# Performance work log

Hardware: AMD Instinct MI355X
Metric: run time of the kernel (lower is better)

The kernel has to match this reference:

```python
import jax, jax.numpy as jnp
import numpy as np

EMBED_DIM = 256
N_HEADS = 8
HEAD_DIM = EMBED_DIM // N_HEADS
SCALE = HEAD_DIM ** -0.5
CLAMP = 50.0


def setup_inputs() -> dict:
    key = jax.random.key(0)
    ks = jax.random.split(key, 5)
    B, R, N, E = 2, 32, 512, EMBED_DIM
    x = jax.random.normal(ks[0], (B, R, N, E), dtype=jnp.float32)
    # key-padding mask, broadcastable to (b, h, i, j): keys >= 448 are masked
    mask = (jnp.arange(N) < 448)[None, None, None, :]
    Wqkv = jax.random.normal(ks[1], (E, 3 * E), dtype=jnp.float32) * (E ** -0.5)
    bqkv = jax.random.normal(ks[2], (3 * E,), dtype=jnp.float32) * 0.02
    Wo = jax.random.normal(ks[3], (E, E), dtype=jnp.float32) * (E ** -0.5)
    bo = jax.random.normal(ks[4], (E,), dtype=jnp.float32) * 0.02
    return {"x": x, "mask": mask, "Wqkv": Wqkv, "bqkv": bqkv, "Wo": Wo, "bo": bo}


def reference(x, mask, Wqkv, bqkv, Wo, bo):
    *lead, n, e = x.shape
    xf = x.reshape(-1, n, e)                        # (b, n, e), b = prod(lead)
    qkv = xf @ Wqkv + bqkv                          # (b, n, 3e)
    q, k, v = jnp.split(qkv, 3, axis=-1)
    def heads(t):                                   # (b, n, e) -> (b, h, n, d)
        return t.reshape(t.shape[0], n, N_HEADS, HEAD_DIM).transpose(0, 2, 1, 3)
    q, k, v = heads(q), heads(k), heads(v)
    attn = jnp.einsum('bhid,bhjd->bhij', q, k) * SCALE
    attn = jnp.clip(attn, -CLAMP, CLAMP)
    attn = jnp.where(mask, attn, -jnp.inf)
    attn = jax.nn.softmax(attn, axis=-1)
    # dropout is identity in eval mode
    out = jnp.einsum('bhij,bhjd->bhid', attn, v)    # (b, h, n, d)
    out = out.transpose(0, 2, 1, 3).reshape(-1, n, e)
    out = out @ Wo + bo
    return out.reshape(*lead, n, e)
```

## Files before the change

kernel.cpp:

```cpp
#include <hip/hip_runtime.h>
#include <hip/hip_bf16.h>


typedef __bf16 bf16x8 __attribute__((ext_vector_type(8)));
typedef float f32x4 __attribute__((ext_vector_type(4)));
typedef __hip_bfloat16 bf16_t;

#define QSCALE 0.2550348762f
#define MAXC   72.13475204444817f

__device__ __forceinline__ bf16_t f2b(float f) { return __float2bfloat16(f); }

__global__ __launch_bounds__(256) void prep_w(
    const float* __restrict__ Wqkv, const float* __restrict__ Wo,
    bf16_t* __restrict__ wq_t, bf16_t* __restrict__ wo_t)
{
    int i = blockIdx.x * 256 + threadIdx.x;
    if (i < 196608) { int n = i >> 8, k = i & 255; wq_t[i] = f2b(Wqkv[k * 768 + n]); }
    else { int j = i - 196608; int n = j >> 8, k = j & 255; wo_t[j] = f2b(Wo[k * 256 + n]); }
}

__global__ __launch_bounds__(256) void qkv_gemm(
    const float* __restrict__ x, const bf16_t* __restrict__ Bt, const float* __restrict__ bias,
    bf16_t* __restrict__ Qp, bf16_t* __restrict__ Kp, bf16_t* __restrict__ Vp)
{
    __shared__ bf16_t smem[2 * 128 * 72];
    bf16_t* As = smem;
    bf16_t* Bs = smem + 128 * 72;
    const int tid = threadIdx.x, lane = tid & 63, w = tid >> 6;
    const int q = lane >> 4, c = lane & 15;
    const int wm = w >> 1, wn = w & 1;
    const int bm0 = blockIdx.x * 128, bn0 = blockIdx.y * 128;

    const f32x4 fz = {0.f, 0.f, 0.f, 0.f};
    f32x4 acc[4][4];
#pragma unroll
    for (int i = 0; i < 4; i++)
#pragma unroll
        for (int j = 0; j < 4; j++) acc[i][j] = fz;

    for (int kk = 0; kk < 4; ++kk) {
        const int k0 = kk * 64;
#pragma unroll
        for (int t = 0; t < 8; t++) {
            int idx = tid + t * 256;
            int row = idx >> 4, c4 = idx & 15;
            float4 f = *(const float4*)&x[(size_t)(bm0 + row) * 256 + k0 + c4 * 4];
            union { ushort4 u; bf16_t h[4]; } pk;
            pk.h[0] = f2b(f.x); pk.h[1] = f2b(f.y); pk.h[2] = f2b(f.z); pk.h[3] = f2b(f.w);
            *(ushort4*)&As[row * 72 + c4 * 4] = pk.u;
        }
#pragma unroll
        for (int t = 0; t < 4; t++) {
            int idx = tid + t * 256;
            int row = idx >> 3, c8 = idx & 7;
            *(uint4*)&Bs[row * 72 + c8 * 8] = *(const uint4*)&Bt[(size_t)(bn0 + row) * 256 + k0 + c8 * 8];
        }
        __syncthreads();
#pragma unroll
        for (int ks = 0; ks < 2; ks++) {
            bf16x8 af[4], bfr[4];
#pragma unroll
            for (int mt = 0; mt < 4; mt++) af[mt] = *(const bf16x8*)&As[(wm * 64 + mt * 16 + c) * 72 + ks * 32 + q * 8];
#pragma unroll
            for (int nt = 0; nt < 4; nt++) bfr[nt] = *(const bf16x8*)&Bs[(wn * 64 + nt * 16 + c) * 72 + ks * 32 + q * 8];
#pragma unroll
            for (int mt = 0; mt < 4; mt++)
#pragma unroll
                for (int nt = 0; nt < 4; nt++)
                    acc[mt][nt] = __builtin_amdgcn_mfma_f32_16x16x32_bf16(af[mt], bfr[nt], acc[mt][nt], 0, 0, 0);
        }
        __syncthreads();
    }

    bf16_t* T = smem + w * 4608;
    const int sel = bn0 >> 8;
    const int npb = bm0 + wm * 64;
    const int bseq = npb >> 9;
    const int blk = (npb & 511) >> 6;
    const int hbase = ((bn0 >> 5) & 7) + wn * 2;

    if (sel == 2) {
#pragma unroll
        for (int mt = 0; mt < 4; mt++)
#pragma unroll
            for (int nt = 0; nt < 4; nt++) {
                int gn = bn0 + wn * 64 + nt * 16 + c;
                float b = bias[gn];
                union { ushort4 u; bf16_t h[4]; } pk;
#pragma unroll
                for (int r = 0; r < 4; r++) pk.h[r] = f2b(acc[mt][nt][r] + b);
                *(ushort4*)&T[(nt * 16 + c) * 72 + mt * 16 + q * 4] = pk.u;
            }
        if (blk < 7) {
#pragma unroll
            for (int t = 0; t < 8; t++) {
                int h = t >> 2, s2 = (t >> 1) & 1, dt = t & 1;
                uint4 vv = *(const uint4*)&T[(h * 32 + dt * 16 + c) * 72 + s2 * 32 + q * 8];
                int bh = bseq * 8 + hbase + h;
                *(uint4*)&Vp[((((size_t)bh * 7 + blk) * 2 + s2) * 2 + dt) * 512 + lane * 8] = vv;
            }
        }
    } else {
        const float sc = (sel == 0) ? QSCALE : 1.0f;
#pragma unroll
        for (int mt = 0; mt < 4; mt++)
#pragma unroll
            for (int nt = 0; nt < 4; nt++) {
                int gn = bn0 + wn * 64 + nt * 16 + c;
                float b = bias[gn];
#pragma unroll
                for (int r = 0; r < 4; r++)
                    T[(mt * 16 + q * 4 + r) * 72 + nt * 16 + c] = f2b((acc[mt][nt][r] + b) * sc);
            }
        if (sel == 0) {
#pragma unroll
            for (int t = 0; t < 8; t++) {
                int h = t >> 2, g = t & 3;
                uint4 vv = *(const uint4*)&T[(g * 16 + c) * 72 + h * 32 + q * 8];
                int bh = bseq * 8 + hbase + h;
                *(uint4*)&Qp[(((size_t)bh * 8 + blk) * 4 + g) * 512 + lane * 8] = vv;
            }
        } else if (blk < 7) {
#pragma unroll
            for (int t = 0; t < 8; t++) {
                int h = t >> 2, g = t & 3;
                uint4 vv = *(const uint4*)&T[(g * 16 + c) * 72 + h * 32 + q * 8];
                int bh = bseq * 8 + hbase + h;
                *(uint4*)&Kp[(((size_t)bh * 7 + blk) * 4 + g) * 512 + lane * 8] = vv;
            }
        }
    }
}

__global__ __launch_bounds__(256) void attn_kernel(
    const bf16_t* __restrict__ Qp, const bf16_t* __restrict__ Kp,
    const bf16_t* __restrict__ Vp, bf16_t* __restrict__ a_buf)
{
    __shared__ bf16_t Pw[4 * 16 * 68];
    const int tid = threadIdx.x, lane = tid & 63, w = tid >> 6;
    const int q = lane >> 4, c = lane & 15;
    const int bh = blockIdx.x & 511, part = blockIdx.x >> 9;
    bf16_t* pw = &Pw[w * 16 * 68];

    bf16x8 Qf = *(const bf16x8*)&Qp[(((size_t)bh * 8 + part) * 4 + w) * 512 + lane * 8];

    union { bf16x8 v; bf16_t h[8]; } ones;
#pragma unroll
    for (int j = 0; j < 8; j++) ones.h[j] = f2b(1.0f);

    const f32x4 fz = {0.f, 0.f, 0.f, 0.f};
    f32x4 O0 = fz, O1 = fz, lacc = fz;

#pragma unroll 1
    for (int ch = 0; ch < 7; ++ch) {
        bf16x8 Kf[4], Vf[4];
#pragma unroll
        for (int nt = 0; nt < 4; nt++)
            Kf[nt] = *(const bf16x8*)&Kp[(((size_t)bh * 7 + ch) * 4 + nt) * 512 + lane * 8];
#pragma unroll
        for (int t = 0; t < 4; t++)
            Vf[t] = *(const bf16x8*)&Vp[(((size_t)bh * 7 + ch) * 4 + t) * 512 + lane * 8];

        f32x4 s[4];
#pragma unroll
        for (int nt = 0; nt < 4; nt++)
            s[nt] = __builtin_amdgcn_mfma_f32_16x16x32_bf16(Qf, Kf[nt], fz, 0, 0, 0);
#pragma unroll
        for (int nt = 0; nt < 4; nt++)
#pragma unroll
            for (int r = 0; r < 4; r++) {
                float t = fminf(s[nt][r] - MAXC, 0.f);
                pw[(q * 4 + r) * 68 + nt * 16 + c] = f2b(__builtin_amdgcn_exp2f(t));
            }
#pragma unroll
        for (int s2 = 0; s2 < 2; s2++) {
            bf16x8 Pa = *(const bf16x8*)&pw[c * 68 + s2 * 32 + q * 8];
            lacc = __builtin_amdgcn_mfma_f32_16x16x32_bf16(Pa, ones.v, lacc, 0, 0, 0);
            O0 = __builtin_amdgcn_mfma_f32_16x16x32_bf16(Pa, Vf[s2 * 2 + 0], O0, 0, 0, 0);
            O1 = __builtin_amdgcn_mfma_f32_16x16x32_bf16(Pa, Vf[s2 * 2 + 1], O1, 0, 0, 0);
        }
    }

    const int bseq = bh >> 3, hh = bh & 7;
#pragma unroll
    for (int r = 0; r < 4; r++) {
        float inv = 1.f / lacc[r];
        int row = part * 64 + w * 16 + q * 4 + r;
        size_t tok = (size_t)bseq * 512 + row;
        a_buf[tok * 256 + hh * 32 + c]      = f2b(O0[r] * inv);
        a_buf[tok * 256 + hh * 32 + 16 + c] = f2b(O1[r] * inv);
    }
}

__global__ __launch_bounds__(256) void out_gemm(
    const bf16_t* __restrict__ A, const bf16_t* __restrict__ Bt, const float* __restrict__ bias,
    float* __restrict__ out)
{
    __shared__ bf16_t As[128 * 72];
    __shared__ bf16_t Bs[64 * 72];
    const int tid = threadIdx.x, lane = tid & 63, w = tid >> 6;
    const int q = lane >> 4, c = lane & 15;
    const int bm0 = blockIdx.x * 128, bn0 = blockIdx.y * 64;

    const f32x4 fz = {0.f, 0.f, 0.f, 0.f};
    f32x4 acc[2][4];
#pragma unroll
    for (int i = 0; i < 2; i++)
#pragma unroll
        for (int j = 0; j < 4; j++) acc[i][j] = fz;

    for (int kk = 0; kk < 4; ++kk) {
        const int k0 = kk * 64;
#pragma unroll
        for (int t = 0; t < 4; t++) {
            int idx = tid + t * 256;
            int row = idx >> 3, c8 = idx & 7;
            *(uint4*)&As[row * 72 + c8 * 8] = *(const uint4*)&A[(size_t)(bm0 + row) * 256 + k0 + c8 * 8];
        }
#pragma unroll
        for (int t = 0; t < 2; t++) {
            int idx = tid + t * 256;
            int row = idx >> 3, c8 = idx & 7;
            *(uint4*)&Bs[row * 72 + c8 * 8] = *(const uint4*)&Bt[(size_t)(bn0 + row) * 256 + k0 + c8 * 8];
        }
        __syncthreads();
#pragma unroll
        for (int ks = 0; ks < 2; ks++) {
            bf16x8 af[2], bfr[4];
#pragma unroll
            for (int mt = 0; mt < 2; mt++) af[mt] = *(const bf16x8*)&As[(w * 32 + mt * 16 + c) * 72 + ks * 32 + q * 8];
#pragma unroll
            for (int nt = 0; nt < 4; nt++) bfr[nt] = *(const bf16x8*)&Bs[(nt * 16 + c) * 72 + ks * 32 + q * 8];
#pragma unroll
            for (int mt = 0; mt < 2; mt++)
#pragma unroll
                for (int nt = 0; nt < 4; nt++)
                    acc[mt][nt] = __builtin_amdgcn_mfma_f32_16x16x32_bf16(af[mt], bfr[nt], acc[mt][nt], 0, 0, 0);
        }
        __syncthreads();
    }
#pragma unroll
    for (int mt = 0; mt < 2; mt++)
#pragma unroll
        for (int nt = 0; nt < 4; nt++) {
            int gn = bn0 + nt * 16 + c;
            float b = bias[gn];
#pragma unroll
            for (int r = 0; r < 4; r++) {
                int gm = bm0 + w * 32 + mt * 16 + q * 4 + r;
                out[(size_t)gm * 256 + gn] = acc[mt][nt][r] + b;
            }
        }
}

extern "C" void kernel_launch(void* const* d_in, const int* in_sizes, int n_in,
                              void* d_out, int out_size, void* d_ws, size_t ws_size,
                              hipStream_t stream)
{
    const float* x    = (const float*)d_in[0];
    const float* Wqkv = (const float*)d_in[2];
    const float* bqkv = (const float*)d_in[3];
    const float* Wo   = (const float*)d_in[4];
    const float* bo   = (const float*)d_in[5];
    float* out = (float*)d_out;

    char* ws = (char*)d_ws;
    bf16_t* Qp    = (bf16_t*)(ws);
    bf16_t* Kp    = (bf16_t*)(ws + 16777216);
    bf16_t* Vp    = (bf16_t*)(ws + 31457280);
    bf16_t* a_buf = (bf16_t*)(ws + 46137344);
    bf16_t* wq_t  = (bf16_t*)(ws + 62914560);
    bf16_t* wo_t  = (bf16_t*)(ws + 63307776);

    prep_w<<<1024, 256, 0, stream>>>(Wqkv, Wo, wq_t, wo_t);
    qkv_gemm<<<dim3(256, 6), 256, 0, stream>>>(x, wq_t, bqkv, Qp, Kp, Vp);
    attn_kernel<<<4096, 256, 0, stream>>>(Qp, Kp, Vp, a_buf);
    out_gemm<<<dim3(256, 4), 256, 0, stream>>>(a_buf, wo_t, bo, out);
}
```

Measured before the change: 171.5 us.

## Fuse output projection into attention kernel with MFMA-fragment-ordered Wo

Merges the attention and output-projection kernels. Each block now handles one sequence's 32 query rows across all 8 heads (two passes of 4 waves), stages the normalized head outputs in shared memory, and runs the Wo GEMM directly from there. Wo is pre-packed in MFMA fragment order so B fragments load straight from global memory. This removes the bf16 a_buf round trip and one kernel launch, but cuts the attention grid from 4096 to 1024 blocks. Each wave now re-reads K/V per head pass and holds two query tiles, which adds register pressure.

```diff
diff --git a/kernel.cpp b/kernel.cpp
--- a/kernel.cpp
+++ b/kernel.cpp
@@ -13,11 +13,18 @@
 
 __global__ __launch_bounds__(256) void prep_w(
     const float* __restrict__ Wqkv, const float* __restrict__ Wo,
-    bf16_t* __restrict__ wq_t, bf16_t* __restrict__ wo_t)
+    bf16_t* __restrict__ wq_t, bf16_t* __restrict__ Wof)
 {
     int i = blockIdx.x * 256 + threadIdx.x;
-    if (i < 196608) { int n = i >> 8, k = i & 255; wq_t[i] = f2b(Wqkv[k * 768 + n]); }
-    else { int j = i - 196608; int n = j >> 8, k = j & 255; wo_t[j] = f2b(Wo[k * 256 + n]); }
+    if (i < 196608) {
+        int n = i >> 8, k = i & 255;
+        wq_t[i] = f2b(Wqkv[k * 768 + n]);
+    } else {
+        int j = i - 196608;
+        int n = j >> 8, k = j & 255;
+        int ks = k >> 5, nt = n >> 4, cc = n & 15, qq = (k >> 3) & 3, jj = k & 7;
+        Wof[(((ks * 16 + nt) * 4 + qq) * 16 + cc) * 8 + jj] = f2b(Wo[k * 256 + n]);
+    }
 }
 
 __global__ __launch_bounds__(256) void qkv_gemm(
@@ -133,123 +140,112 @@
     }
 }
 
-__global__ __launch_bounds__(256) void attn_kernel(
+__global__ __launch_bounds__(256) void attn_fused(
     const bf16_t* __restrict__ Qp, const bf16_t* __restrict__ Kp,
-    const bf16_t* __restrict__ Vp, bf16_t* __restrict__ a_buf)
-{
+    const bf16_t* __restrict__ Vp, const bf16_t* __restrict__ Wof,
+    const float* __restrict__ bo, float* __restrict__ out)
+{
+    __shared__ bf16_t Os[32 * 280];
     __shared__ bf16_t Pw[4 * 16 * 68];
     const int tid = threadIdx.x, lane = tid & 63, w = tid >> 6;
     const int q = lane >> 4, c = lane & 15;
-    const int bh = blockIdx.x & 511, part = blockIdx.x >> 9;
+    const int b = blockIdx.x;
+    const int seq = b & 63, part = b >> 6;
     bf16_t* pw = &Pw[w * 16 * 68];
 
-    bf16x8 Qf = *(const bf16x8*)&Qp[(((size_t)bh * 8 + part) * 4 + w) * 512 + lane * 8];
-
     union { bf16x8 v; bf16_t h[8]; } ones;
 #pragma unroll
     for (int j = 0; j < 8; j++) ones.h[j] = f2b(1.0f);
-
     const f32x4 fz = {0.f, 0.f, 0.f, 0.f};
-    f32x4 O0 = fz, O1 = fz, lacc = fz;
 
 #pragma unroll 1
-    for (int ch = 0; ch < 7; ++ch) {
-        bf16x8 Kf[4], Vf[4];
-#pragma unroll
-        for (int nt = 0; nt < 4; nt++)
-            Kf[nt] = *(const bf16x8*)&Kp[(((size_t)bh * 7 + ch) * 4 + nt) * 512 + lane * 8];
-#pragma unroll
-        for (int t = 0; t < 4; t++)
-            Vf[t] = *(const bf16x8*)&Vp[(((size_t)bh * 7 + ch) * 4 + t) * 512 + lane * 8];
-
-        f32x4 s[4];
-#pragma unroll
-        for (int nt = 0; nt < 4; nt++)
-            s[nt] = __builtin_amdgcn_mfma_f32_16x16x32_bf16(Qf, Kf[nt], fz, 0, 0, 0);
-#pragma unroll
-        for (int nt = 0; nt < 4; nt++)
+    for (int pass = 0; pass < 2; ++pass) {
+        const int head = w + pass * 4;
+        const int bh = seq * 8 + head;
+
+        bf16x8 Qf[2];
+#pragma unroll
+        for (int mt = 0; mt < 2; mt++)
+            Qf[mt] = *(const bf16x8*)&Qp[(((size_t)bh * 8 + (part >> 1)) * 4 + (part & 1) * 2 + mt) * 512 + lane * 8];
+
+        f32x4 O[2][2], lacc[2];
+#pragma unroll
+        for (int mt = 0; mt < 2; mt++) { O[mt][0] = fz; O[mt][1] = fz; lacc[mt] = fz; }
+
+#pragma unroll 1
+        for (int ch = 0; ch < 7; ++ch) {
+            bf16x8 Kf[4], Vf[4];
+#pragma unroll
+            for (int nt = 0; nt < 4; nt++)
+                Kf[nt] = *(const bf16x8*)&Kp[(((size_t)bh * 7 + ch) * 4 + nt) * 512 + lane * 8];
+#pragma unroll
+            for (int t = 0; t < 4; t++)
+                Vf[t] = *(const bf16x8*)&Vp[(((size_t)bh * 7 + ch) * 4 + t) * 512 + lane * 8];
+
+#pragma unroll
+            for (int mt = 0; mt < 2; mt++) {
+                f32x4 s[4];
+#pragma unroll
+                for (int nt = 0; nt < 4; nt++)
+                    s[nt] = __builtin_amdgcn_mfma_f32_16x16x32_bf16(Qf[mt], Kf[nt], fz, 0, 0, 0);
+#pragma unroll
+                for (int nt = 0; nt < 4; nt++)
+#pragma unroll
+                    for (int r = 0; r < 4; r++) {
+                        float t = fminf(s[nt][r] - MAXC, 0.f);
+                        pw[(q * 4 + r) * 68 + nt * 16 + c] = f2b(__builtin_amdgcn_exp2f(t));
+                    }
+#pragma unroll
+                for (int s2 = 0; s2 < 2; s2++) {
+                    bf16x8 Pa = *(const bf16x8*)&pw[c * 68 + s2 * 32 + q * 8];
+                    lacc[mt] = __builtin_amdgcn_mfma_f32_16x16x32_bf16(Pa, ones.v, lacc[mt], 0, 0, 0);
+                    O[mt][0] = __builtin_amdgcn_mfma_f32_16x16x32_bf16(Pa, Vf[s2 * 2 + 0], O[mt][0], 0, 0, 0);
+                    O[mt][1] = __builtin_amdgcn_mfma_f32_16x16x32_bf16(Pa, Vf[s2 * 2 + 1], O[mt][1], 0, 0, 0);
+                }
+            }
+        }
+#pragma unroll
+        for (int mt = 0; mt < 2; mt++)
 #pragma unroll
             for (int r = 0; r < 4; r++) {
-                float t = fminf(s[nt][r] - MAXC, 0.f);
-                pw[(q * 4 + r) * 68 + nt * 16 + c] = f2b(__builtin_amdgcn_exp2f(t));
-            }
-#pragma unroll
-        for (int s2 = 0; s2 < 2; s2++) {
-            bf16x8 Pa = *(const bf16x8*)&pw[c * 68 + s2 * 32 + q * 8];
-            lacc = __builtin_amdgcn_mfma_f32_16x16x32_bf16(Pa, ones.v, lacc, 0, 0, 0);
-            O0 = __builtin_amdgcn_mfma_f32_16x16x32_bf16(Pa, Vf[s2 * 2 + 0], O0, 0, 0, 0);
-            O1 = __builtin_amdgcn_mfma_f32_16x16x32_bf16(Pa, Vf[s2 * 2 + 1], O1, 0, 0, 0);
-        }
-    }
-
-    const int bseq = bh >> 3, hh = bh & 7;
-#pragma unroll
-    for (int r = 0; r < 4; r++) {
-        float inv = 1.f / lacc[r];
-        int row = part * 64 + w * 16 + q * 4 + r;
-        size_t tok = (size_t)bseq * 512 + row;
-        a_buf[tok * 256 + hh * 32 + c]      = f2b(O0[r] * inv);
-        a_buf[tok * 256 + hh * 32 + 16 + c] = f2b(O1[r] * inv);
-    }
-}
-
-__global__ __launch_bounds__(256) void out_gemm(
-    const bf16_t* __restrict__ A, const bf16_t* __restrict__ Bt, const float* __restrict__ bias,
-    float* __restrict__ out)
-{
-    __shared__ bf16_t As[128 * 72];
-    __shared__ bf16_t Bs[64 * 72];
-    const int tid = threadIdx.x, lane = tid & 63, w = tid >> 6;
-    const int q = lane >> 4, c = lane & 15;
-    const int bm0 = blockIdx.x * 128, bn0 = blockIdx.y * 64;
-
-    const f32x4 fz = {0.f, 0.f, 0.f, 0.f};
+                float inv = 1.f / lacc[mt][r];
+                int row = mt * 16 + q * 4 + r;
+                Os[row * 280 + head * 32 + c]      = f2b(O[mt][0][r] * inv);
+                Os[row * 280 + head * 32 + 16 + c] = f2b(O[mt][1][r] * inv);
+            }
+    }
+    __syncthreads();
+
     f32x4 acc[2][4];
 #pragma unroll
     for (int i = 0; i < 2; i++)
 #pragma unroll
         for (int j = 0; j < 4; j++) acc[i][j] = fz;
 
-    for (int kk = 0; kk < 4; ++kk) {
-        const int k0 = kk * 64;
-#pragma unroll
-        for (int t = 0; t < 4; t++) {
-            int idx = tid + t * 256;
-            int row = idx >> 3, c8 = idx & 7;
-            *(uint4*)&As[row * 72 + c8 * 8] = *(const uint4*)&A[(size_t)(bm0 + row) * 256 + k0 + c8 * 8];
-        }
-#pragma unroll
-        for (int t = 0; t < 2; t++) {
-            int idx = tid + t * 256;
-            int row = idx >> 3, c8 = idx & 7;
-            *(uint4*)&Bs[row * 72 + c8 * 8] = *(const uint4*)&Bt[(size_t)(bn0 + row) * 256 + k0 + c8 * 8];
-        }
-        __syncthreads();
-#pragma unroll
-        for (int ks = 0; ks < 2; ks++) {
-            bf16x8 af[2], bfr[4];
-#pragma unroll
-            for (int mt = 0; mt < 2; mt++) af[mt] = *(const bf16x8*)&As[(w * 32 + mt * 16 + c) * 72 + ks * 32 + q * 8];
-#pragma unroll
-            for (int nt = 0; nt < 4; nt++) bfr[nt] = *(const bf16x8*)&Bs[(nt * 16 + c) * 72 + ks * 32 + q * 8];
+#pragma unroll
+    for (int ks = 0; ks < 8; ++ks) {
+        bf16x8 af[2];
+#pragma unroll
+        for (int mt = 0; mt < 2; mt++)
+            af[mt] = *(const bf16x8*)&Os[(mt * 16 + c) * 280 + ks * 32 + q * 8];
+#pragma unroll
+        for (int nt = 0; nt < 4; nt++) {
+            bf16x8 bfr = *(const bf16x8*)&Wof[(((size_t)ks * 16 + w * 4 + nt) * 64 + lane) * 8];
 #pragma unroll
             for (int mt = 0; mt < 2; mt++)
-#pragma unroll
-                for (int nt = 0; nt < 4; nt++)
-                    acc[mt][nt] = __builtin_amdgcn_mfma_f32_16x16x32_bf16(af[mt], bfr[nt], acc[mt][nt], 0, 0, 0);
-        }
-        __syncthreads();
+                acc[mt][nt] = __builtin_amdgcn_mfma_f32_16x16x32_bf16(af[mt], bfr, acc[mt][nt], 0, 0, 0);
+        }
     }
 #pragma unroll
     for (int mt = 0; mt < 2; mt++)
 #pragma unroll
         for (int nt = 0; nt < 4; nt++) {
-            int gn = bn0 + nt * 16 + c;
-            float b = bias[gn];
+            int gn = w * 64 + nt * 16 + c;
+            float bb = bo[gn];
 #pragma unroll
             for (int r = 0; r < 4; r++) {
-                int gm = bm0 + w * 32 + mt * 16 + q * 4 + r;
-                out[(size_t)gm * 256 + gn] = acc[mt][nt][r] + b;
+                int gm = seq * 512 + part * 32 + mt * 16 + q * 4 + r;
+                out[(size_t)gm * 256 + gn] = acc[mt][nt][r] + bb;
             }
         }
 }
@@ -266,15 +262,13 @@
     float* out = (float*)d_out;
 
     char* ws = (char*)d_ws;
-    bf16_t* Qp    = (bf16_t*)(ws);
-    bf16_t* Kp    = (bf16_t*)(ws + 16777216);
-    bf16_t* Vp    = (bf16_t*)(ws + 31457280);
-    bf16_t* a_buf = (bf16_t*)(ws + 46137344);
-    bf16_t* wq_t  = (bf16_t*)(ws + 62914560);
-    bf16_t* wo_t  = (bf16_t*)(ws + 63307776);
-
-    prep_w<<<1024, 256, 0, stream>>>(Wqkv, Wo, wq_t, wo_t);
+    bf16_t* Qp   = (bf16_t*)(ws);
+    bf16_t* Kp   = (bf16_t*)(ws + 16777216);
+    bf16_t* Vp   = (bf16_t*)(ws + 31457280);
+    bf16_t* wq_t = (bf16_t*)(ws + 46137344);
+    bf16_t* Wof  = (bf16_t*)(ws + 46530560);
+
+    prep_w<<<1024, 256, 0, stream>>>(Wqkv, Wo, wq_t, Wof);
     qkv_gemm<<<dim3(256, 6), 256, 0, stream>>>(x, wq_t, bqkv, Qp, Kp, Vp);
-    attn_kernel<<<4096, 256, 0, stream>>>(Qp, Kp, Vp, a_buf);
-    out_gemm<<<dim3(256, 4), 256, 0, stream>>>(a_buf, wo_t, bo, out);
-}
+    attn_fused<<<1024, 256, 0, stream>>>(Qp, Kp, Vp, Wof, bo, out);
+}
```

Measured after the change: 169.7 us. No clear change (-1.0%).
